# Performance work log

Measured on AMD Instinct MI355X. Metric: run time of the kernel, lower is better.

Reference implementation:

```python
import jax, jax.numpy as jnp
import numpy as np

N_NODES = 100_000
N_EDGES = 3_200_000
F_IN, HID, OUT = 64, 64, 6


def setup_inputs() -> dict:
    key = jax.random.key(0)
    k1, k2, k3, k4 = jax.random.split(key, 4)
    x = jax.random.normal(k1, (N_NODES, F_IN), dtype=jnp.float32)
    edge_index = jax.random.randint(k2, (2, N_EDGES), 0, N_NODES, dtype=jnp.int32)
    W1 = jax.random.normal(k3, (F_IN, HID), dtype=jnp.float32) * (1.0 / np.sqrt(F_IN))
    b1 = jnp.zeros((HID,), dtype=jnp.float32)
    W2 = jax.random.normal(k4, (HID, OUT), dtype=jnp.float32) * (1.0 / np.sqrt(HID))
    b2 = jnp.zeros((OUT,), dtype=jnp.float32)
    return {"x": x, "edge_index": edge_index, "W1": W1, "b1": b1, "W2": W2, "b2": b2}


def _gcn_conv(x, row, col, norm, W, b):
    # x: [N, F_in], row/col/norm: [E'], W: [F_in, F_out]
    n = x.shape[0]
    h = x @ W                                   # [N, F_out]
    msg = h[row] * norm[:, None]                # gather + scale, [E', F_out]
    out = jax.ops.segment_sum(msg, col, num_segments=n)  # scatter-add to targets
    return out + b


def reference(x, edge_index, W1, b1, W2, b2):
    n = x.shape[0]
    # add self-loops (PyG GCNConv default)
    loops = jnp.arange(n, dtype=edge_index.dtype)
    row = jnp.concatenate([edge_index[0], loops])  # source
    col = jnp.concatenate([edge_index[1], loops])  # target
    # symmetric normalization: deg computed at target incl. self-loops
    deg = jax.ops.segment_sum(jnp.ones_like(col, dtype=x.dtype), col, num_segments=n)
    dinv = jnp.where(deg > 0, jax.lax.rsqrt(deg), 0.0)
    norm = dinv[row] * dinv[col]                # [E']

    h = jax.nn.relu(_gcn_conv(x, row, col, norm, W1, b1))
    out = _gcn_conv(h, row, col, norm, W2, b2)
    return jnp.mean(out, axis=0)                # [OUT]
```

## Files before the change

### kernel.cpp

```cpp
#include <hip/hip_runtime.h>

#define N_NODES 100000
#define N_EDGES 3200000
#define NOUT 6

#define NPB 256
#define NBUK ((N_NODES + NPB - 1) / NPB)
#define CAP 12288
#define PCHUNK 4096
#define PNB ((N_EDGES + PCHUNK - 1) / PCHUNK)
#define SORT_CAP 10240
#define AGB (N_NODES / 32)
#define NPART (2 * AGB)

typedef __attribute__((ext_vector_type(2))) float v2f;

#if defined(__has_builtin)
#if __has_builtin(__builtin_amdgcn_cvt_scalef32_pk_f32_fp4) && __has_builtin(__builtin_amdgcn_cvt_scalef32_pk_fp4_f32)
#define USE_FP4 1
#endif
#endif
#ifndef USE_FP4
#define USE_FP4 0
#endif

__global__ __launch_bounds__(512) void k_partition(const int* __restrict__ row,
                                                   const int* __restrict__ col,
                                                   int* __restrict__ gcursor,
                                                   int* __restrict__ bedge) {
    __shared__ int hist[512];
    __shared__ int lstart[512];
    __shared__ int lcur[512];
    __shared__ int gbase[512];
    __shared__ int sscan[512];
    __shared__ int stage[PCHUNK];
    __shared__ unsigned short stageb[PCHUNK];

    const int t = threadIdx.x;
    const int c0 = blockIdx.x * PCHUNK;
    int cnt = N_EDGES - c0; if (cnt > PCHUNK) cnt = PCHUNK;

    hist[t] = 0; lcur[t] = 0;
    __syncthreads();

    int myp[8]; int myb[8];
#pragma unroll
    for (int i = 0; i < 8; ++i) {
        int p = i * 512 + t;
        myb[i] = -1;
        if (p < cnt) {
            int e = c0 + p;
            int c = col[e], r = row[e];
            int b = c >> 8;
            myp[i] = ((c & 255) << 17) | r;
            myb[i] = b;
            atomicAdd(&hist[b], 1);
        }
    }
    __syncthreads();

    int hv = hist[t];
    sscan[t] = hv;
    __syncthreads();
    for (int off = 1; off < 512; off <<= 1) {
        int u = (t >= off) ? sscan[t - off] : 0;
        __syncthreads();
        sscan[t] += u;
        __syncthreads();
    }
    lstart[t] = sscan[t] - hv;
    if (t < NBUK && hv > 0) gbase[t] = atomicAdd(&gcursor[t], hv);
    __syncthreads();

#pragma unroll
    for (int i = 0; i < 8; ++i) {
        if (myb[i] >= 0) {
            int pos = lstart[myb[i]] + atomicAdd(&lcur[myb[i]], 1);
            stage[pos] = myp[i];
            stageb[pos] = (unsigned short)myb[i];
        }
    }
    __syncthreads();

    for (int p = t; p < cnt; p += 512) {
        int b = stageb[p];
        int rel = gbase[b] + p - lstart[b];
        if (rel < CAP) bedge[b * CAP + rel] = stage[p];
    }
}

__global__ __launch_bounds__(512) void k_bucket_sort(const int* __restrict__ gcursor,
                                                     const int* __restrict__ bedge,
                                                     float* __restrict__ dinv,
                                                     int* __restrict__ node_off,
                                                     int* __restrict__ sorted_row) {
    __shared__ int cnt[NPB];
    __shared__ int lstart[NPB];
    __shared__ int lcur[NPB];
    __shared__ int sc[NPB];
    __shared__ int stage[SORT_CAP];

    const int t = threadIdx.x;
    const int b = blockIdx.x;
    const int s = b * CAP;
    int m = gcursor[b]; if (m > CAP) m = CAP;
    const bool fits = (m <= SORT_CAP);

    if (t < NPB) { cnt[t] = 0; lcur[t] = 0; }
    __syncthreads();

    if (fits) {
        for (int j = t; j < m; j += 512) {
            int p = bedge[s + j];
            stage[j] = p;
            atomicAdd(&cnt[p >> 17], 1);
        }
    } else {
        for (int j = t; j < m; j += 512) atomicAdd(&cnt[bedge[s + j] >> 17], 1);
    }
    __syncthreads();

    if (t < NPB) sc[t] = cnt[t];
    __syncthreads();
    for (int off = 1; off < NPB; off <<= 1) {
        int u = 0;
        if (t < NPB && t >= off) u = sc[t - off];
        __syncthreads();
        if (t < NPB && t >= off) sc[t] += u;
        __syncthreads();
    }
    if (t < NPB) {
        int c = cnt[t];
        lstart[t] = sc[t] - c;
        node_off[b * 257 + t] = s + sc[t] - c;
        int g = b * NPB + t;
        if (g < N_NODES) dinv[g] = rsqrtf((float)c + 1.0f);
    }
    if (t == 256) node_off[b * 257 + 256] = s + m;
    __syncthreads();

    if (fits) {
        for (int j = t; j < m; j += 512) {
            int p = stage[j];
            int lc = p >> 17;
            int pos = lstart[lc] + atomicAdd(&lcur[lc], 1);
            sorted_row[s + pos] = p & 0x1FFFF;
        }
    } else {
        for (int j = t; j < m; j += 512) {
            int p = bedge[s + j];
            int lc = p >> 17;
            int pos = lstart[lc] + atomicAdd(&lcur[lc], 1);
            sorted_row[s + pos] = p & 0x1FFFF;
        }
    }
}

__global__ __launch_bounds__(256) void k_gemm1(const float* __restrict__ x,
                                               const float* __restrict__ W1,
                                               const float* __restrict__ dinv,
                                               unsigned int* __restrict__ hs1b) {
    __shared__ float Ws[64 * 64];
    __shared__ float Xs[64 * 65];
    const int tx = threadIdx.x;
    const int nodeBase = blockIdx.x * 64;

    for (int t = tx; t < 64 * 64; t += 256) Ws[t] = W1[t];

    for (int t = tx; t < 64 * 16; t += 256) {
        int r = t >> 4, c4 = t & 15;
        int g = nodeBase + r;
        float4 v = make_float4(0.f, 0.f, 0.f, 0.f);
        if (g < N_NODES) v = reinterpret_cast<const float4*>(x)[g * 16 + c4];
        float* p = &Xs[r * 65 + c4 * 4];
        p[0] = v.x; p[1] = v.y; p[2] = v.z; p[3] = v.w;
    }
    __syncthreads();

    const int nG = tx >> 4;
    const int cG = tx & 15;
    float acc[4][4] = {};
    for (int k = 0; k < 64; ++k) {
        float4 w = *reinterpret_cast<const float4*>(&Ws[k * 64 + cG * 4]);
#pragma unroll
        for (int i = 0; i < 4; ++i) {
            float xv = Xs[(nG * 4 + i) * 65 + k];
            acc[i][0] = fmaf(xv, w.x, acc[i][0]);
            acc[i][1] = fmaf(xv, w.y, acc[i][1]);
            acc[i][2] = fmaf(xv, w.z, acc[i][2]);
            acc[i][3] = fmaf(xv, w.w, acc[i][3]);
        }
    }

#pragma unroll
    for (int i = 0; i < 4; ++i) {
        int n = nodeBase + nG * 4 + i;
        if (n < N_NODES) {
            float dv = dinv[n];
#if USE_FP4
            unsigned int u = 0;
            u = __builtin_amdgcn_cvt_scalef32_pk_fp4_f32(u, acc[i][0] * dv * 8.0f, acc[i][1] * dv * 8.0f, 1.0f, 0);
            u = __builtin_amdgcn_cvt_scalef32_pk_fp4_f32(u, acc[i][2] * dv * 8.0f, acc[i][3] * dv * 8.0f, 1.0f, 1);
            reinterpret_cast<unsigned short*>(hs1b)[n * 16 + cG] = (unsigned short)(u & 0xFFFFu);
#else
            int u = __builtin_amdgcn_cvt_pk_fp8_f32(acc[i][0] * dv, acc[i][1] * dv, 0, false);
            u = __builtin_amdgcn_cvt_pk_fp8_f32(acc[i][2] * dv, acc[i][3] * dv, u, true);
            hs1b[n * 16 + cG] = (unsigned int)u;
#endif
        }
    }
}

#if USE_FP4
__device__ inline void addrow4(float* __restrict__ acc, unsigned int u) {
    v2f p0 = __builtin_amdgcn_cvt_scalef32_pk_f32_fp4(u, 1.0f, 0);
    v2f p1 = __builtin_amdgcn_cvt_scalef32_pk_f32_fp4(u, 1.0f, 1);
    v2f p2 = __builtin_amdgcn_cvt_scalef32_pk_f32_fp4(u, 1.0f, 2);
    v2f p3 = __builtin_amdgcn_cvt_scalef32_pk_f32_fp4(u, 1.0f, 3);
    acc[0] += p0.x; acc[1] += p0.y; acc[2] += p1.x; acc[3] += p1.y;
    acc[4] += p2.x; acc[5] += p2.y; acc[6] += p3.x; acc[7] += p3.y;
}
#else
__device__ inline void addrow8(float* __restrict__ acc, uint2 u) {
    v2f p0 = __builtin_amdgcn_cvt_pk_f32_fp8((int)u.x, false);
    v2f p1 = __builtin_amdgcn_cvt_pk_f32_fp8((int)u.x, true);
    v2f p2 = __builtin_amdgcn_cvt_pk_f32_fp8((int)u.y, false);
    v2f p3 = __builtin_amdgcn_cvt_pk_f32_fp8((int)u.y, true);
    acc[0] += p0.x; acc[1] += p0.y; acc[2] += p1.x; acc[3] += p1.y;
    acc[4] += p2.x; acc[5] += p2.y; acc[6] += p3.x; acc[7] += p3.y;
}
#endif

__global__ __launch_bounds__(256) void k_agg_l2(const int* __restrict__ node_off,
                                                const int* __restrict__ sorted_row,
                                                const unsigned int* __restrict__ hs1b,
                                                const float* __restrict__ W2,
                                                const float* __restrict__ b1,
                                                const float* __restrict__ dinv,
                                                float* __restrict__ hs2,
                                                float* __restrict__ partials) {
    __shared__ float W2s[64 * NOUT];
    __shared__ float b1s[64];
    __shared__ float pacc[8];
    const int tx = threadIdx.x;
    for (int t = tx; t < 64 * NOUT; t += 256) W2s[t] = W2[t];
    if (tx < 64) b1s[tx] = b1[tx];
    if (tx < 8) pacc[tx] = 0.f;
    __syncthreads();

    const int node = (blockIdx.x * 256 + tx) >> 3;
    const int l = tx & 7;
    const int idx = (node >> 8) * 257 + (node & 255);
    const int s = node_off[idx], e = node_off[idx + 1];

    float acc[8] = {};
#if USE_FP4
    const unsigned int* h1 = hs1b;
    addrow4(acc, h1[node * 8 + l]);
    int j = s;
    for (; j + 8 <= e; j += 8) {
        int r0 = __builtin_nontemporal_load(&sorted_row[j]);
        int r1 = __builtin_nontemporal_load(&sorted_row[j + 1]);
        int r2 = __builtin_nontemporal_load(&sorted_row[j + 2]);
        int r3 = __builtin_nontemporal_load(&sorted_row[j + 3]);
        int r4 = __builtin_nontemporal_load(&sorted_row[j + 4]);
        int r5 = __builtin_nontemporal_load(&sorted_row[j + 5]);
        int r6 = __builtin_nontemporal_load(&sorted_row[j + 6]);
        int r7 = __builtin_nontemporal_load(&sorted_row[j + 7]);
        unsigned int g0 = h1[r0 * 8 + l], g1 = h1[r1 * 8 + l];
        unsigned int g2 = h1[r2 * 8 + l], g3 = h1[r3 * 8 + l];
        unsigned int g4 = h1[r4 * 8 + l], g5 = h1[r5 * 8 + l];
        unsigned int g6 = h1[r6 * 8 + l], g7 = h1[r7 * 8 + l];
        addrow4(acc, g0); addrow4(acc, g1); addrow4(acc, g2); addrow4(acc, g3);
        addrow4(acc, g4); addrow4(acc, g5); addrow4(acc, g6); addrow4(acc, g7);
    }
    for (; j < e; ++j) addrow4(acc, h1[__builtin_nontemporal_load(&sorted_row[j]) * 8 + l]);
    const float dv = dinv[node];
    const float dva = dv * 0.125f;
#else
    const uint2* h8 = reinterpret_cast<const uint2*>(hs1b);
    addrow8(acc, h8[node * 8 + l]);
    int j = s;
    for (; j + 4 <= e; j += 4) {
        int r0 = __builtin_nontemporal_load(&sorted_row[j]);
        int r1 = __builtin_nontemporal_load(&sorted_row[j + 1]);
        int r2 = __builtin_nontemporal_load(&sorted_row[j + 2]);
        int r3 = __builtin_nontemporal_load(&sorted_row[j + 3]);
        uint2 a = h8[r0 * 8 + l];
        uint2 b = h8[r1 * 8 + l];
        uint2 c = h8[r2 * 8 + l];
        uint2 d = h8[r3 * 8 + l];
        addrow8(acc, a); addrow8(acc, b); addrow8(acc, c); addrow8(acc, d);
    }
    for (; j < e; ++j) addrow8(acc, h8[__builtin_nontemporal_load(&sorted_row[j]) * 8 + l]);
    const float dv = dinv[node];
    const float dva = dv;
#endif

    float sj[NOUT] = {};
#pragma unroll
    for (int i = 0; i < 8; ++i) {
        float hv = fmaxf(fmaf(dva, acc[i], b1s[l * 8 + i]), 0.f);
#pragma unroll
        for (int q = 0; q < NOUT; ++q) sj[q] = fmaf(hv, W2s[(l * 8 + i) * NOUT + q], sj[q]);
    }
#pragma unroll
    for (int q = 0; q < NOUT; ++q) {
        sj[q] += __shfl_xor(sj[q], 1, 64);
        sj[q] += __shfl_xor(sj[q], 2, 64);
        sj[q] += __shfl_xor(sj[q], 4, 64);
    }
    if (l == 0) {
        float4 o0 = make_float4(sj[0] * dv, sj[1] * dv, sj[2] * dv, sj[3] * dv);
        float4 o1 = make_float4(sj[4] * dv, sj[5] * dv, 0.f, 0.f);
        reinterpret_cast<float4*>(hs2)[node * 2] = o0;
        reinterpret_cast<float4*>(hs2)[node * 2 + 1] = o1;
        float sc = dv * dv;
#pragma unroll
        for (int q = 0; q < NOUT; ++q) atomicAdd(&pacc[q], sj[q] * sc);
    }
    __syncthreads();
    if (tx < NOUT) partials[blockIdx.x * 8 + tx] = pacc[tx];
}

__global__ __launch_bounds__(256) void k_wsum2(const int* __restrict__ node_off,
                                               const int* __restrict__ sorted_row,
                                               const float* __restrict__ dinv,
                                               const float* __restrict__ hs2,
                                               float* __restrict__ partials) {
    const int tx = threadIdx.x;
    const int node = (blockIdx.x * 256 + tx) >> 3;
    const int l = tx & 7;
    const int idx = (node >> 8) * 257 + (node & 255);
    const int s = node_off[idx], e = node_off[idx + 1];

    float a = 0.f;
    int j = s;
    for (; j + 4 <= e; j += 4) {
        int r0 = __builtin_nontemporal_load(&sorted_row[j]);
        int r1 = __builtin_nontemporal_load(&sorted_row[j + 1]);
        int r2 = __builtin_nontemporal_load(&sorted_row[j + 2]);
        int r3 = __builtin_nontemporal_load(&sorted_row[j + 3]);
        float f0 = hs2[r0 * 8 + l];
        float f1 = hs2[r1 * 8 + l];
        float f2 = hs2[r2 * 8 + l];
        float f3 = hs2[r3 * 8 + l];
        a += (f0 + f1) + (f2 + f3);
    }
    for (; j < e; ++j) a += hs2[__builtin_nontemporal_load(&sorted_row[j]) * 8 + l];
    a *= dinv[node];

    a += __shfl_xor(a, 8, 64);
    a += __shfl_xor(a, 16, 64);
    a += __shfl_xor(a, 32, 64);
    __shared__ float wred[4][8];
    const int lane = tx & 63, w = tx >> 6;
    if (lane < 8) wred[w][lane] = a;
    __syncthreads();
    if (tx < 8)
        partials[(AGB + blockIdx.x) * 8 + tx] = wred[0][tx] + wred[1][tx] + wred[2][tx] + wred[3][tx];
}

__global__ __launch_bounds__(256) void k_reduce2(const float* __restrict__ partials,
                                                 const float* __restrict__ b2,
                                                 float* __restrict__ out) {
    __shared__ float s[256];
    for (int j = 0; j < NOUT; ++j) {
        float a = 0.f;
        for (int p = threadIdx.x; p < NPART; p += 256) a += partials[p * 8 + j];
        s[threadIdx.x] = a;
        __syncthreads();
        for (int off = 128; off > 0; off >>= 1) {
            if (threadIdx.x < off) s[threadIdx.x] += s[threadIdx.x + off];
            __syncthreads();
        }
        if (threadIdx.x == 0) out[j] = b2[j] + s[0] * (1.0f / N_NODES);
        __syncthreads();
    }
}

extern "C" void kernel_launch(void* const* d_in, const int* in_sizes, int n_in,
                              void* d_out, int out_size, void* d_ws, size_t ws_size,
                              hipStream_t stream) {
    const float* x  = (const float*)d_in[0];
    const int*   ei = (const int*)d_in[1];
    const float* W1 = (const float*)d_in[2];
    const float* b1 = (const float*)d_in[3];
    const float* W2 = (const float*)d_in[4];
    const float* b2 = (const float*)d_in[5];
    float* out = (float*)d_out;

    unsigned int* hs1b = (unsigned int*)d_ws;
    float* dinv      = (float*)(hs1b + 1600000);
    float* hs2       = dinv + 100352;
    float* partials  = hs2 + 800000;
    int*   gcursor   = (int*)(partials + 50176);
    int*   node_off  = gcursor + 512;
    int*   sorted_row= node_off + 100864;
    int*   bedge     = sorted_row + 4804608;

    const int* row = ei;
    const int* col = ei + N_EDGES;

    hipMemsetAsync(gcursor, 0, NBUK * sizeof(int), stream);
    k_partition<<<PNB, 512, 0, stream>>>(row, col, gcursor, bedge);
    k_bucket_sort<<<NBUK, 512, 0, stream>>>(gcursor, bedge, dinv, node_off, sorted_row);

    k_gemm1<<<(N_NODES + 63) / 64, 256, 0, stream>>>(x, W1, dinv, hs1b);

    k_agg_l2<<<AGB, 256, 0, stream>>>(node_off, sorted_row, hs1b, W2, b1, dinv, hs2, partials);

    k_wsum2<<<AGB, 256, 0, stream>>>(node_off, sorted_row, dinv, hs2, partials);

    k_reduce2<<<1, 256, 0, stream>>>(partials, b2, out);
}
```

Before: 194.7 us.

## Fuse GEMM1 into bucket sort and software-pipeline edge gathers with shuffled indices

```diff
diff --git a/kernel.cpp b/kernel.cpp
--- a/kernel.cpp
+++ b/kernel.cpp
@@ -23,6 +23,11 @@
 #ifndef USE_FP4
 #define USE_FP4 0
 #endif
+
+__global__ __launch_bounds__(512) void k_initcur(int* __restrict__ gcursor) {
+    int t = threadIdx.x;
+    if (t < NBUK) gcursor[t] = 0;
+}
 
 __global__ __launch_bounds__(512) void k_partition(const int* __restrict__ row,
                                                    const int* __restrict__ col,
@@ -89,15 +94,19 @@
     }
 }
 
-__global__ __launch_bounds__(512) void k_bucket_sort(const int* __restrict__ gcursor,
-                                                     const int* __restrict__ bedge,
-                                                     float* __restrict__ dinv,
-                                                     int* __restrict__ node_off,
-                                                     int* __restrict__ sorted_row) {
+__global__ __launch_bounds__(512) void k_sortgemm(const int* __restrict__ gcursor,
+                                                  const int* __restrict__ bedge,
+                                                  const float* __restrict__ x,
+                                                  const float* __restrict__ W1,
+                                                  float* __restrict__ dinv,
+                                                  int* __restrict__ node_off,
+                                                  int* __restrict__ sorted_row,
+                                                  unsigned int* __restrict__ hs1b) {
     __shared__ int cnt[NPB];
     __shared__ int lstart[NPB];
     __shared__ int lcur[NPB];
     __shared__ int sc[NPB];
+    __shared__ float fdinv[NPB];
     __shared__ int stage[SORT_CAP];
 
     const int t = threadIdx.x;
@@ -133,8 +142,10 @@
         int c = cnt[t];
         lstart[t] = sc[t] - c;
         node_off[b * 257 + t] = s + sc[t] - c;
+        float dv = rsqrtf((float)c + 1.0f);
+        fdinv[t] = dv;
         int g = b * NPB + t;
-        if (g < N_NODES) dinv[g] = rsqrtf((float)c + 1.0f);
+        if (g < N_NODES) dinv[g] = dv;
     }
     if (t == 256) node_off[b * 257 + 256] = s + m;
     __syncthreads();
@@ -154,59 +165,58 @@
             sorted_row[s + pos] = p & 0x1FFFF;
         }
     }
-}
-
-__global__ __launch_bounds__(256) void k_gemm1(const float* __restrict__ x,
-                                               const float* __restrict__ W1,
-                                               const float* __restrict__ dinv,
-                                               unsigned int* __restrict__ hs1b) {
-    __shared__ float Ws[64 * 64];
-    __shared__ float Xs[64 * 65];
-    const int tx = threadIdx.x;
-    const int nodeBase = blockIdx.x * 64;
-
-    for (int t = tx; t < 64 * 64; t += 256) Ws[t] = W1[t];
-
-    for (int t = tx; t < 64 * 16; t += 256) {
-        int r = t >> 4, c4 = t & 15;
-        int g = nodeBase + r;
-        float4 v = make_float4(0.f, 0.f, 0.f, 0.f);
-        if (g < N_NODES) v = reinterpret_cast<const float4*>(x)[g * 16 + c4];
-        float* p = &Xs[r * 65 + c4 * 4];
-        p[0] = v.x; p[1] = v.y; p[2] = v.z; p[3] = v.w;
-    }
-    __syncthreads();
-
-    const int nG = tx >> 4;
-    const int cG = tx & 15;
-    float acc[4][4] = {};
-    for (int k = 0; k < 64; ++k) {
-        float4 w = *reinterpret_cast<const float4*>(&Ws[k * 64 + cG * 4]);
-#pragma unroll
-        for (int i = 0; i < 4; ++i) {
-            float xv = Xs[(nG * 4 + i) * 65 + k];
-            acc[i][0] = fmaf(xv, w.x, acc[i][0]);
-            acc[i][1] = fmaf(xv, w.y, acc[i][1]);
-            acc[i][2] = fmaf(xv, w.z, acc[i][2]);
-            acc[i][3] = fmaf(xv, w.w, acc[i][3]);
-        }
-    }
-
-#pragma unroll
-    for (int i = 0; i < 4; ++i) {
-        int n = nodeBase + nG * 4 + i;
-        if (n < N_NODES) {
-            float dv = dinv[n];
+    __syncthreads();
+
+    float* Ws = (float*)stage;
+    float* Xs = ((float*)stage) + 4096;
+
+    for (int i = t; i < 1024; i += 512)
+        reinterpret_cast<float4*>(Ws)[i] = reinterpret_cast<const float4*>(W1)[i];
+
+    const int nG = t >> 4;
+    const int cG = t & 15;
+    for (int sub = 0; sub < 4; ++sub) {
+        const int nodeBase = b * NPB + sub * 64;
+        __syncthreads();
+        for (int i = t; i < 1024; i += 512) {
+            int r = i >> 4, c4 = i & 15;
+            int g = nodeBase + r;
+            float4 v = make_float4(0.f, 0.f, 0.f, 0.f);
+            if (g < N_NODES) v = reinterpret_cast<const float4*>(x)[g * 16 + c4];
+            float* p = &Xs[r * 65 + c4 * 4];
+            p[0] = v.x; p[1] = v.y; p[2] = v.z; p[3] = v.w;
+        }
+        __syncthreads();
+
+        float acc[2][4] = {};
+        for (int k = 0; k < 64; ++k) {
+            float4 w = *reinterpret_cast<const float4*>(&Ws[k * 64 + cG * 4]);
+#pragma unroll
+            for (int i = 0; i < 2; ++i) {
+                float xv = Xs[(nG * 2 + i) * 65 + k];
+                acc[i][0] = fmaf(xv, w.x, acc[i][0]);
+                acc[i][1] = fmaf(xv, w.y, acc[i][1]);
+                acc[i][2] = fmaf(xv, w.z, acc[i][2]);
+                acc[i][3] = fmaf(xv, w.w, acc[i][3]);
+            }
+        }
+#pragma unroll
+        for (int i = 0; i < 2; ++i) {
+            int loc = sub * 64 + nG * 2 + i;
+            int n = b * NPB + loc;
+            if (n < N_NODES) {
+                float dv = fdinv[loc];
 #if USE_FP4
-            unsigned int u = 0;
-            u = __builtin_amdgcn_cvt_scalef32_pk_fp4_f32(u, acc[i][0] * dv * 8.0f, acc[i][1] * dv * 8.0f, 1.0f, 0);
-            u = __builtin_amdgcn_cvt_scalef32_pk_fp4_f32(u, acc[i][2] * dv * 8.0f, acc[i][3] * dv * 8.0f, 1.0f, 1);
-            reinterpret_cast<unsigned short*>(hs1b)[n * 16 + cG] = (unsigned short)(u & 0xFFFFu);
+                unsigned int u = 0;
+                u = __builtin_amdgcn_cvt_scalef32_pk_fp4_f32(u, acc[i][0] * dv * 8.0f, acc[i][1] * dv * 8.0f, 1.0f, 0);
+                u = __builtin_amdgcn_cvt_scalef32_pk_fp4_f32(u, acc[i][2] * dv * 8.0f, acc[i][3] * dv * 8.0f, 1.0f, 1);
+                reinterpret_cast<unsigned short*>(hs1b)[n * 16 + cG] = (unsigned short)(u & 0xFFFFu);
 #else
-            int u = __builtin_amdgcn_cvt_pk_fp8_f32(acc[i][0] * dv, acc[i][1] * dv, 0, false);
-            u = __builtin_amdgcn_cvt_pk_fp8_f32(acc[i][2] * dv, acc[i][3] * dv, u, true);
-            hs1b[n * 16 + cG] = (unsigned int)u;
-#endif
+                int u = __builtin_amdgcn_cvt_pk_fp8_f32(acc[i][0] * dv, acc[i][1] * dv, 0, false);
+                u = __builtin_amdgcn_cvt_pk_fp8_f32(acc[i][2] * dv, acc[i][3] * dv, u, true);
+                hs1b[n * 16 + cG] = (unsigned int)u;
+#endif
+            }
         }
     }
 }
@@ -220,6 +230,9 @@
     acc[0] += p0.x; acc[1] += p0.y; acc[2] += p1.x; acc[3] += p1.y;
     acc[4] += p2.x; acc[5] += p2.y; acc[6] += p3.x; acc[7] += p3.y;
 }
+#define GATHER_T unsigned int
+#define GATHER(hsrc, r, l) (hsrc)[(r) * 8 + (l)]
+#define CONSUME(acc, g) addrow4(acc, g)
 #else
 __device__ inline void addrow8(float* __restrict__ acc, uint2 u) {
     v2f p0 = __builtin_amdgcn_cvt_pk_f32_fp8((int)u.x, false);
@@ -229,6 +242,9 @@
     acc[0] += p0.x; acc[1] += p0.y; acc[2] += p1.x; acc[3] += p1.y;
     acc[4] += p2.x; acc[5] += p2.y; acc[6] += p3.x; acc[7] += p3.y;
 }
+#define GATHER_T uint2
+#define GATHER(hsrc, r, l) (hsrc)[(r) * 8 + (l)]
+#define CONSUME(acc, g) addrow8(acc, g)
 #endif
 
 __global__ __launch_bounds__(256) void k_agg_l2(const int* __restrict__ node_off,
@@ -250,50 +266,74 @@
 
     const int node = (blockIdx.x * 256 + tx) >> 3;
     const int l = tx & 7;
+    const int gb = tx & 56;
     const int idx = (node >> 8) * 257 + (node & 255);
     const int s = node_off[idx], e = node_off[idx + 1];
 
+#if USE_FP4
+    const unsigned int* hsrc = hs1b;
+#else
+    const uint2* hsrc = reinterpret_cast<const uint2*>(hs1b);
+#endif
+
     float acc[8] = {};
+    CONSUME(acc, GATHER(hsrc, node, l));
+    int j = s;
+    const int nb = (e - s) >> 3;
+    if (nb >= 2) {
+        int idxA = sorted_row[j + l];
+        GATHER_T gv[8];
+#pragma unroll
+        for (int k = 0; k < 8; ++k) {
+            int rk = __shfl(idxA, gb + k, 64);
+            gv[k] = GATHER(hsrc, rk, l);
+        }
+        int idxB = sorted_row[j + 8 + l];
+        for (int bi = 2; bi < nb; ++bi) {
+            int idxC = sorted_row[j + bi * 8 + l];
+            GATHER_T nv[8];
+#pragma unroll
+            for (int k = 0; k < 8; ++k) {
+                int rk = __shfl(idxB, gb + k, 64);
+                nv[k] = GATHER(hsrc, rk, l);
+            }
+#pragma unroll
+            for (int k = 0; k < 8; ++k) CONSUME(acc, gv[k]);
+#pragma unroll
+            for (int k = 0; k < 8; ++k) gv[k] = nv[k];
+            idxB = idxC;
+        }
+        {
+            GATHER_T nv[8];
+#pragma unroll
+            for (int k = 0; k < 8; ++k) {
+                int rk = __shfl(idxB, gb + k, 64);
+                nv[k] = GATHER(hsrc, rk, l);
+            }
+#pragma unroll
+            for (int k = 0; k < 8; ++k) CONSUME(acc, gv[k]);
+#pragma unroll
+            for (int k = 0; k < 8; ++k) CONSUME(acc, nv[k]);
+        }
+        j += nb * 8;
+    } else if (nb == 1) {
+        int idxA = sorted_row[j + l];
+        GATHER_T gv[8];
+#pragma unroll
+        for (int k = 0; k < 8; ++k) {
+            int rk = __shfl(idxA, gb + k, 64);
+            gv[k] = GATHER(hsrc, rk, l);
+        }
+#pragma unroll
+        for (int k = 0; k < 8; ++k) CONSUME(acc, gv[k]);
+        j += 8;
+    }
+    for (; j < e; ++j) CONSUME(acc, GATHER(hsrc, sorted_row[j], l));
+
+    const float dv = dinv[node];
 #if USE_FP4
-    const unsigned int* h1 = hs1b;
-    addrow4(acc, h1[node * 8 + l]);
-    int j = s;
-    for (; j + 8 <= e; j += 8) {
-        int r0 = __builtin_nontemporal_load(&sorted_row[j]);
-        int r1 = __builtin_nontemporal_load(&sorted_row[j + 1]);
-        int r2 = __builtin_nontemporal_load(&sorted_row[j + 2]);
-        int r3 = __builtin_nontemporal_load(&sorted_row[j + 3]);
-        int r4 = __builtin_nontemporal_load(&sorted_row[j + 4]);
-        int r5 = __builtin_nontemporal_load(&sorted_row[j + 5]);
-        int r6 = __builtin_nontemporal_load(&sorted_row[j + 6]);
-        int r7 = __builtin_nontemporal_load(&sorted_row[j + 7]);
-        unsigned int g0 = h1[r0 * 8 + l], g1 = h1[r1 * 8 + l];
-        unsigned int g2 = h1[r2 * 8 + l], g3 = h1[r3 * 8 + l];
-        unsigned int g4 = h1[r4 * 8 + l], g5 = h1[r5 * 8 + l];
-        unsigned int g6 = h1[r6 * 8 + l], g7 = h1[r7 * 8 + l];
-        addrow4(acc, g0); addrow4(acc, g1); addrow4(acc, g2); addrow4(acc, g3);
-        addrow4(acc, g4); addrow4(acc, g5); addrow4(acc, g6); addrow4(acc, g7);
-    }
-    for (; j < e; ++j) addrow4(acc, h1[__builtin_nontemporal_load(&sorted_row[j]) * 8 + l]);
-    const float dv = dinv[node];
     const float dva = dv * 0.125f;
 #else
-    const uint2* h8 = reinterpret_cast<const uint2*>(hs1b);
-    addrow8(acc, h8[node * 8 + l]);
-    int j = s;
-    for (; j + 4 <= e; j += 4) {
-        int r0 = __builtin_nontemporal_load(&sorted_row[j]);
-        int r1 = __builtin_nontemporal_load(&sorted_row[j + 1]);
-        int r2 = __builtin_nontemporal_load(&sorted_row[j + 2]);
-        int r3 = __builtin_nontemporal_load(&sorted_row[j + 3]);
-        uint2 a = h8[r0 * 8 + l];
-        uint2 b = h8[r1 * 8 + l];
-        uint2 c = h8[r2 * 8 + l];
-        uint2 d = h8[r3 * 8 + l];
-        addrow8(acc, a); addrow8(acc, b); addrow8(acc, c); addrow8(acc, d);
-    }
-    for (; j < e; ++j) addrow8(acc, h8[__builtin_nontemporal_load(&sorted_row[j]) * 8 + l]);
-    const float dv = dinv[node];
     const float dva = dv;
 #endif
 
@@ -331,23 +371,56 @@
     const int tx = threadIdx.x;
     const int node = (blockIdx.x * 256 + tx) >> 3;
     const int l = tx & 7;
+    const int gb = tx & 56;
     const int idx = (node >> 8) * 257 + (node & 255);
     const int s = node_off[idx], e = node_off[idx + 1];
 
     float a = 0.f;
     int j = s;
-    for (; j + 4 <= e; j += 4) {
-        int r0 = __builtin_nontemporal_load(&sorted_row[j]);
-        int r1 = __builtin_nontemporal_load(&sorted_row[j + 1]);
-        int r2 = __builtin_nontemporal_load(&sorted_row[j + 2]);
-        int r3 = __builtin_nontemporal_load(&sorted_row[j + 3]);
-        float f0 = hs2[r0 * 8 + l];
-        float f1 = hs2[r1 * 8 + l];
-        float f2 = hs2[r2 * 8 + l];
-        float f3 = hs2[r3 * 8 + l];
-        a += (f0 + f1) + (f2 + f3);
-    }
-    for (; j < e; ++j) a += hs2[__builtin_nontemporal_load(&sorted_row[j]) * 8 + l];
+    const int nb = (e - s) >> 3;
+    if (nb >= 2) {
+        int idxA = sorted_row[j + l];
+        float gv[8];
+#pragma unroll
+        for (int k = 0; k < 8; ++k) {
+            int rk = __shfl(idxA, gb + k, 64);
+            gv[k] = hs2[rk * 8 + l];
+        }
+        int idxB = sorted_row[j + 8 + l];
+        for (int bi = 2; bi < nb; ++bi) {
+            int idxC = sorted_row[j + bi * 8 + l];
+            float nv[8];
+#pragma unroll
+            for (int k = 0; k < 8; ++k) {
+                int rk = __shfl(idxB, gb + k, 64);
+                nv[k] = hs2[rk * 8 + l];
+            }
+            a += ((gv[0] + gv[1]) + (gv[2] + gv[3])) + ((gv[4] + gv[5]) + (gv[6] + gv[7]));
+#pragma unroll
+            for (int k = 0; k < 8; ++k) gv[k] = nv[k];
+            idxB = idxC;
+        }
+        {
+            float nv[8];
+#pragma unroll
+            for (int k = 0; k < 8; ++k) {
+                int rk = __shfl(idxB, gb + k, 64);
+                nv[k] = hs2[rk * 8 + l];
+            }
+            a += ((gv[0] + gv[1]) + (gv[2] + gv[3])) + ((gv[4] + gv[5]) + (gv[6] + gv[7]));
+            a += ((nv[0] + nv[1]) + (nv[2] + nv[3])) + ((nv[4] + nv[5]) + (nv[6] + nv[7]));
+        }
+        j += nb * 8;
+    } else if (nb == 1) {
+        int idxA = sorted_row[j + l];
+#pragma unroll
+        for (int k = 0; k < 8; ++k) {
+            int rk = __shfl(idxA, gb + k, 64);
+            a += hs2[rk * 8 + l];
+        }
+        j += 8;
+    }
+    for (; j < e; ++j) a += hs2[sorted_row[j] * 8 + l];
     a *= dinv[node];
 
     a += __shfl_xor(a, 8, 64);
@@ -402,11 +475,9 @@
     const int* row = ei;
     const int* col = ei + N_EDGES;
 
-    hipMemsetAsync(gcursor, 0, NBUK * sizeof(int), stream);
+    k_initcur<<<1, 512, 0, stream>>>(gcursor);
     k_partition<<<PNB, 512, 0, stream>>>(row, col, gcursor, bedge);
-    k_bucket_sort<<<NBUK, 512, 0, stream>>>(gcursor, bedge, dinv, node_off, sorted_row);
-
-    k_gemm1<<<(N_NODES + 63) / 64, 256, 0, stream>>>(x, W1, dinv, hs1b);
+    k_sortgemm<<<NBUK, 512, 0, stream>>>(gcursor, bedge, x, W1, dinv, node_off, sorted_row, hs1b);
 
     k_agg_l2<<<AGB, 256, 0, stream>>>(node_off, sorted_row, hs1b, W2, b1, dinv, hs2, partials);
 
```

New measurement: 325.6 us. 1.67x slower.
